# Kernel optimization log

Hardware: AMD Instinct MI355X
Metric: run time of the kernel (lower is better)

## Reference

```python
import jax, jax.numpy as jnp
import numpy as np

NHEAD = 8
ROUTING_STEPS = 2
TEMP = 1.0
ROPE_THETA = 10000.0


def rmsnorm(x, w, eps=1e-6):
    return x * jax.lax.rsqrt(jnp.mean(x * x, axis=-1, keepdims=True) + eps) * w


def rope_cos_sin(seq_len, head_dim, theta):
    inv = 1.0 / (theta ** (jnp.arange(0, head_dim, 2, dtype=jnp.float32) / head_dim))
    freqs = jnp.outer(jnp.arange(seq_len, dtype=jnp.float32), inv)  # [S, hd/2]
    return jnp.cos(freqs), jnp.sin(freqs)


def apply_rope(x, cos, sin):
    # x: [B,H,S,hd]; cos/sin: [S, hd/2]
    x1, x2 = x[..., 0::2], x[..., 1::2]
    c, s = cos[None, None], sin[None, None]
    r1 = x1 * c - x2 * s
    r2 = x1 * s + x2 * c
    return jnp.stack([r1, r2], axis=-1).reshape(x.shape)


def cube_forward(x, wq, wk, wv, wo, w1, w2, g1, g2, cos, sin):
    # Per-sample gathered expert weights: wq.. [B,D,D], w1 [B,D,F], w2 [B,F,D]
    B, S, D = x.shape
    H = NHEAD
    hd = D // H
    xn = rmsnorm(x, g1[:, None, :])
    q = jnp.einsum('bsd,bde->bse', xn, wq).reshape(B, S, H, hd).transpose(0, 2, 1, 3)
    k = jnp.einsum('bsd,bde->bse', xn, wk).reshape(B, S, H, hd).transpose(0, 2, 1, 3)
    v = jnp.einsum('bsd,bde->bse', xn, wv).reshape(B, S, H, hd).transpose(0, 2, 1, 3)
    q = apply_rope(q, cos, sin)
    k = apply_rope(k, cos, sin)
    scores = jnp.einsum('bhqd,bhkd->bhqk', q, k) / jnp.sqrt(jnp.float32(hd))
    causal = jnp.tril(jnp.ones((S, S), dtype=bool))
    scores = jnp.where(causal, scores, jnp.float32(-1e30))
    att = jax.nn.softmax(scores, axis=-1)
    o = jnp.einsum('bhqk,bhkd->bhqd', att, v).transpose(0, 2, 1, 3).reshape(B, S, D)
    x = x + jnp.einsum('bsd,bde->bse', o, wo)
    hn = rmsnorm(x, g2[:, None, :])
    ff = jax.nn.silu(jnp.einsum('bsd,bdf->bsf', hn, w1))
    return x + jnp.einsum('bsf,bfd->bsd', ff, w2)


def reference(input_ids, start_cubes, emb, Wq, Wk, Wv, Wo, W1, W2, n1, n2, gate_w, final_norm_w, fc_out_w):
    B, S = input_ids.shape
    D = emb.shape[1]
    C = Wq.shape[0]
    x = emb[input_ids] * jnp.sqrt(jnp.float32(D))
    cos, sin = rope_cos_sin(S, D // NHEAD, ROPE_THETA)
    # deterministic ring graph: neighbors of cube i are (i+1)%C and (i+2)%C
    ar = jnp.arange(C)
    adj = jnp.zeros((C, C), dtype=bool).at[ar, (ar + 1) % C].set(True).at[ar, (ar + 2) % C].set(True)
    cur = start_cubes
    acc_probs = jnp.zeros(C + 1, dtype=jnp.float32)
    acc_lb = jnp.float32(0.0)
    for _ in range(ROUTING_STEPS):
        x = cube_forward(x, Wq[cur], Wk[cur], Wv[cur], Wo[cur], W1[cur], W2[cur], n1[cur], n2[cur], cos, sin)
        pooled = x.mean(axis=1)                        # [B, D]
        scores = pooled @ gate_w                       # [B, C+1]
        probs = jax.nn.softmax(scores / TEMP, axis=-1)
        acc_probs = acc_probs + probs.sum(axis=0)
        avg = probs.mean(axis=0)
        acc_lb = acc_lb + (C + 1) * jnp.sum(avg * avg)
        masked = jnp.where(adj[cur], scores[:, :C], jnp.float32(-1e30))
        cur = jnp.argmax(masked, axis=-1)
    logits = jnp.einsum('bsd,dv->bsv', rmsnorm(x, final_norm_w), fc_out_w)
    avg_probs = acc_probs / jnp.float32(ROUTING_STEPS * B)
    aux_variance_loss = jnp.var(avg_probs)
    aux_lb_loss = acc_lb / jnp.float32(ROUTING_STEPS)
    return logits, aux_variance_loss, aux_lb_loss


def setup_inputs() -> dict:
    key = jax.random.key(0)
    ks = jax.random.split(key, 16)
    V, D, F, C, B, S = 32000, 512, 2048, 4, 2, 256
    w = 0.02
    return {
        'input_ids': jax.random.randint(ks[0], (B, S), 0, V),
        'start_cubes': jax.random.randint(ks[1], (B,), 0, C),
        'emb': jax.random.normal(ks[2], (V, D), jnp.float32) * w,
        'Wq': jax.random.normal(ks[3], (C, D, D), jnp.float32) * w,
        'Wk': jax.random.normal(ks[4], (C, D, D), jnp.float32) * w,
        'Wv': jax.random.normal(ks[5], (C, D, D), jnp.float32) * w,
        'Wo': jax.random.normal(ks[6], (C, D, D), jnp.float32) * w,
        'W1': jax.random.normal(ks[7], (C, D, F), jnp.float32) * w,
        'W2': jax.random.normal(ks[8], (C, F, D), jnp.float32) * w,
        'n1': jnp.ones((C, D), jnp.float32),
        'n2': jnp.ones((C, D), jnp.float32),
        'gate_w': jax.random.normal(ks[9], (D, C + 1), jnp.float32) * w,
        'final_norm_w': jnp.ones((D,), jnp.float32),
        'fc_out_w': jax.random.normal(ks[10], (D, V), jnp.float32) * w,
    }
```

## Files before the change

### kernel.cpp

```cpp
#include <hip/hip_runtime.h>
#include <hip/hip_bf16.h>

#define BB 2
#define SS 256
#define DDIM 512
#define HH 8
#define HDIM 64
#define FDIM 2048
#define CC 4
#define VV 32000
#define NTOK (BB*SS)
#define PCHUNK 16

typedef __hip_bfloat16 bf16;
typedef __attribute__((ext_vector_type(8))) short short8;
typedef __attribute__((ext_vector_type(4))) short short4v;
typedef __attribute__((ext_vector_type(4))) float floatx4;

__device__ __forceinline__ int get_mode(const unsigned* __restrict__ probe) {
    return (probe[0] == 0x3F800000u) ? 0 : 1;
}
__device__ __forceinline__ float ldw(const void* __restrict__ p, long i, int mode) {
    if (mode == 0) return ((const float*)p)[i];
    return __bfloat162float(((const bf16*)p)[i]);
}
__device__ __forceinline__ void stf(void* __restrict__ p, long i, float v, int mode) {
    if (mode == 0) ((float*)p)[i] = v;
    else ((bf16*)p)[i] = __float2bfloat16(v);
}

__device__ __forceinline__ void gload16(const void* g, void* l) {
    __builtin_amdgcn_global_load_lds(
        (const __attribute__((address_space(1))) unsigned int*)g,
        (__attribute__((address_space(3))) unsigned int*)l, 16, 0, 0);
}

__global__ void init_kernel(const int* __restrict__ ids,
                            const int* __restrict__ start_cubes,
                            const void* __restrict__ emb,
                            float* __restrict__ x,
                            float* __restrict__ acc_probs,
                            float* __restrict__ acc_lb,
                            int* __restrict__ cur,
                            const unsigned* __restrict__ probe) {
    int mode = get_mode(probe);
    int gid = blockIdx.x * blockDim.x + threadIdx.x;
    if (gid < NTOK * DDIM) {
        int tok = gid / DDIM, d = gid % DDIM;
        x[gid] = ldw(emb, (long)ids[tok] * DDIM + d, mode) * 22.627416997969522f;
    }
    if (gid < CC + 1) acc_probs[gid] = 0.f;
    if (gid == CC + 1) *acc_lb = 0.f;
    if (gid < BB) cur[gid] = start_cubes[gid];
}

__global__ void rmsnorm_kernel(const float* __restrict__ in,
                               void* __restrict__ out, int obf,
                               const void* __restrict__ gamma,
                               const int* __restrict__ cur,
                               float* __restrict__ zbuf, int zn,
                               const unsigned* __restrict__ probe) {
    int mode = get_mode(probe);
    int tok = blockIdx.x;
    int b = tok / SS;
    long goff = cur ? (long)cur[b] * DDIM : 0;
    if (zbuf) {
        int gtid = blockIdx.x * blockDim.x + threadIdx.x;
        int gstride = gridDim.x * blockDim.x;
        for (int i = gtid; i < zn; i += gstride) zbuf[i] = 0.f;
    }
    __shared__ float red[256];
    int t = threadIdx.x;
    float x0 = in[(long)tok * DDIM + t];
    float x1 = in[(long)tok * DDIM + t + 256];
    red[t] = x0 * x0 + x1 * x1;
    __syncthreads();
    for (int s = 128; s > 0; s >>= 1) {
        if (t < s) red[t] += red[t + s];
        __syncthreads();
    }
    float scale = rsqrtf(red[0] / DDIM + 1e-6f);
    float v0 = x0 * scale * ldw(gamma, goff + t, mode);
    float v1 = x1 * scale * ldw(gamma, goff + t + 256, mode);
    if (obf) {
        ((bf16*)out)[(long)tok * DDIM + t]       = __float2bfloat16(v0);
        ((bf16*)out)[(long)tok * DDIM + t + 256] = __float2bfloat16(v1);
    } else {
        ((float*)out)[(long)tok * DDIM + t]       = v0;
        ((float*)out)[(long)tok * DDIM + t + 256] = v1;
    }
}

__global__ void silu_kernel(const float* __restrict__ in,
                            ushort* __restrict__ out, int n) {
    int i4 = (blockIdx.x * blockDim.x + threadIdx.x) * 4;
    if (i4 >= n) return;
    float4 v = *(const float4*)&in[i4];
    float a = v.x / (1.f + expf(-v.x));
    float b = v.y / (1.f + expf(-v.y));
    float c = v.z / (1.f + expf(-v.z));
    float d = v.w / (1.f + expf(-v.w));
    bf16 t0 = __float2bfloat16(a), t1 = __float2bfloat16(b);
    bf16 t2 = __float2bfloat16(c), t3 = __float2bfloat16(d);
    short4v o;
    o[0] = *(short*)&t0; o[1] = *(short*)&t1;
    o[2] = *(short*)&t2; o[3] = *(short*)&t3;
    *(short4v*)&out[i4] = o;
}

__global__ void transpose_kernel(const void* __restrict__ in, bf16* __restrict__ out,
                                 int K, int N, long ims, long oms,
                                 const unsigned* __restrict__ probe) {
    int mode = get_mode(probe);
    __shared__ float tile[32][33];
    int mat = blockIdx.z;
    int n0 = blockIdx.x * 32, k0 = blockIdx.y * 32;
    int tx = threadIdx.x, ty = threadIdx.y;
#pragma unroll
    for (int i = 0; i < 4; i++)
        tile[ty + i * 8][tx] = ldw(in, (long)mat * ims + (long)(k0 + ty + i * 8) * N + (n0 + tx), mode);
    __syncthreads();
#pragma unroll
    for (int i = 0; i < 4; i++)
        out[(long)mat * oms + (long)(n0 + ty + i * 8) * K + (k0 + tx)] =
            __float2bfloat16(tile[tx][ty + i * 8]);
}

__global__ __launch_bounds__(256)
void gemm_mfma(const ushort* __restrict__ A,
               const ushort* __restrict__ WtB,
               const int* __restrict__ cur, long wcube, long wz,
               int K, int N,
               const float* __restrict__ res,
               void* __restrict__ out, long ozstride,
               int omode, int ACT, int nsplit, int swz,
               const unsigned* __restrict__ probe) {
    int mode = get_mode(probe);
    __shared__ __align__(16) ushort sA[2][128 * 32];
    __shared__ __align__(16) ushort sB[2][128 * 32];
    int tid = threadIdx.x;
    int mi = blockIdx.y, ni = blockIdx.x;
    if (swz) {
        int nb = gridDim.x, mb = gridDim.y;
        int lin = blockIdx.x + blockIdx.y * nb;
        int nwg = nb * mb;
        int q = nwg >> 3;
        int xcd = lin & 7, pos = lin >> 3;
        int nid = xcd * q + pos;
        mi = nid % mb;
        ni = nid / mb;
    }
    int m0 = mi * 128;
    int n0 = ni * 128;
    int z  = blockIdx.z / nsplit;
    int ks = blockIdx.z % nsplit;
    int Kc = K / nsplit;
    int kbeg = ks * Kc;
    const ushort* Wt = WtB + (long)z * wz + (cur ? (long)cur[m0 / SS] * wcube : 0);
    floatx4 acc[4][4];
#pragma unroll
    for (int i = 0; i < 4; i++)
#pragma unroll
        for (int j = 0; j < 4; j++)
#pragma unroll
            for (int r = 0; r < 4; r++) acc[i][j][r] = 0.f;
    int w = tid >> 6, lane = tid & 63;
    int wm = (w & 1) * 64, wn = (w >> 1) * 64;
    int lr = lane & 15, quad = lane >> 4;

    auto stage = [&](int buf, int k0) {
#pragma unroll
        for (int i = 0; i < 2; i++) {
            int g  = tid + i * 256;
            int gs = g ^ ((g >> 3) & 7);
            int rs = gs >> 2, cs = (gs & 3) * 8;
            gload16(&A[(long)(m0 + rs) * K + k0 + cs],  &sA[buf][g * 8]);
            gload16(&Wt[(long)(n0 + rs) * K + k0 + cs], &sB[buf][g * 8]);
        }
    };

    int nsteps = Kc >> 5;
    stage(0, kbeg);
    for (int j = 0; j < nsteps; ++j) {
        int cu = j & 1;
        if (j + 1 < nsteps) {
            stage(cu ^ 1, kbeg + ((j + 1) << 5));
            asm volatile("s_waitcnt vmcnt(4)" ::: "memory");
        } else {
            asm volatile("s_waitcnt vmcnt(0)" ::: "memory");
        }
        __builtin_amdgcn_sched_barrier(0);
        __builtin_amdgcn_s_barrier();
        short8 af[4], bfr[4];
#pragma unroll
        for (int i = 0; i < 4; i++) {
            int oA = (wm + i * 16 + lr) * 4 + quad;
            int sa = oA ^ ((oA >> 3) & 7);
            af[i]  = *(const short8*)&sA[cu][sa * 8];
            int oB = (wn + i * 16 + lr) * 4 + quad;
            int sb = oB ^ ((oB >> 3) & 7);
            bfr[i] = *(const short8*)&sB[cu][sb * 8];
        }
#pragma unroll
        for (int mm = 0; mm < 4; mm++)
#pragma unroll
            for (int nn = 0; nn < 4; nn++)
                acc[mm][nn] = __builtin_amdgcn_mfma_f32_16x16x32_bf16(af[mm], bfr[nn], acc[mm][nn], 0, 0, 0);
        asm volatile("s_waitcnt lgkmcnt(0)" ::: "memory");
        __builtin_amdgcn_sched_barrier(0);
        __builtin_amdgcn_s_barrier();
    }
#pragma unroll
    for (int mm = 0; mm < 4; mm++)
#pragma unroll
        for (int nn = 0; nn < 4; nn++) {
            int col = n0 + wn + nn * 16 + lr;
#pragma unroll
            for (int r = 0; r < 4; r++) {
                int row = m0 + wm + mm * 16 + quad * 4 + r;
                float v = acc[mm][nn][r];
                long oi = (long)z * ozstride + (long)row * N + col;
                if (omode == 3) {
                    atomicAdd((float*)out + oi, v);
                } else {
                    if (ACT == 1) v = v / (1.f + expf(-v));
                    if (res) v += res[(long)row * N + col];
                    if (omode == 0)      ((float*)out)[oi] = v;
                    else if (omode == 1) ((bf16*)out)[oi] = __float2bfloat16(v);
                    else                 stf(out, oi, v, mode);
                }
            }
        }
}

__global__ void rope_kernel(float* __restrict__ q, float* __restrict__ k) {
    int gid = blockIdx.x * blockDim.x + threadIdx.x;
    if (gid >= NTOK * HH * (HDIM / 2)) return;
    int j = gid % (HDIM / 2);
    int rest = gid / (HDIM / 2);
    int h = rest % HH;
    int tok = rest / HH;
    int s = tok % SS;
    float inv = expf(-(float)j * (logf(10000.f) / 32.f));
    float ang = (float)s * inv;
    float c = cosf(ang), sn = sinf(ang);
    long base = (long)tok * DDIM + h * HDIM + 2 * j;
    float q1 = q[base], q2 = q[base + 1];
    q[base]     = q1 * c - q2 * sn;
    q[base + 1] = q1 * sn + q2 * c;
    float k1 = k[base], k2 = k[base + 1];
    k[base]     = k1 * c - k2 * sn;
    k[base + 1] = k1 * sn + k2 * c;
}

__global__ void attn_kernel(const float* __restrict__ q,
                            const float* __restrict__ k,
                            const float* __restrict__ v,
                            void* __restrict__ o, int obf) {
    int blk = blockIdx.x;
    int qr = blk % SS;
    int h = (blk / SS) % HH;
    int b = blk / (SS * HH);
    int t = threadIdx.x;
    __shared__ float sc[256];
    __shared__ float red[256];
    __shared__ __align__(16) float qs[HDIM];
    long qbase = ((long)(b * SS + qr)) * DDIM + h * HDIM;
    if (t < HDIM) qs[t] = q[qbase + t];
    __syncthreads();
    float s = -1e30f;
    if (t <= qr) {
        long kbase = ((long)(b * SS + t)) * DDIM + h * HDIM;
        const float4* k4 = (const float4*)&k[kbase];
        const float4* q4 = (const float4*)qs;
        float acc = 0.f;
#pragma unroll
        for (int i = 0; i < HDIM / 4; i++) {
            float4 a = q4[i], bv = k4[i];
            acc += a.x * bv.x + a.y * bv.y + a.z * bv.z + a.w * bv.w;
        }
        s = acc * 0.125f;
    }
    sc[t] = s;
    red[t] = s;
    __syncthreads();
    for (int st = 128; st > 0; st >>= 1) {
        if (t < st) red[t] = fmaxf(red[t], red[t + st]);
        __syncthreads();
    }
    float m = red[0];
    __syncthreads();
    float e = (t <= qr) ? expf(sc[t] - m) : 0.f;
    sc[t] = e;
    red[t] = e;
    __syncthreads();
    for (int st = 128; st > 0; st >>= 1) {
        if (t < st) red[t] += red[t + st];
        __syncthreads();
    }
    float invsum = 1.f / red[0];
    __syncthreads();
    int g = t >> 6, d = t & 63;
    float pacc = 0.f;
    for (int kk = g; kk <= qr; kk += 4)
        pacc += sc[kk] * v[((long)(b * SS + kk)) * DDIM + h * HDIM + d];
    red[t] = pacc;
    __syncthreads();
    if (t < HDIM) {
        float vv = (red[t] + red[t + 64] + red[t + 128] + red[t + 192]) * invsum;
        if (obf) ((bf16*)o)[qbase + t] = __float2bfloat16(vv);
        else     ((float*)o)[qbase + t] = vv;
    }
}

__global__ void pool_partial_kernel(const float* __restrict__ x,
                                    float* __restrict__ partial) {
    int blk = blockIdx.x;
    int b = blk / (SS / PCHUNK);
    int c = blk % (SS / PCHUNK);
    int t = threadIdx.x;
    float acc = 0.f;
    long base = ((long)b * SS + c * PCHUNK) * DDIM + t;
#pragma unroll
    for (int i = 0; i < PCHUNK; i++) acc += x[base + (long)i * DDIM];
    partial[(long)blk * DDIM + t] = acc;
}

__global__ void routing_kernel(const float* __restrict__ partial,
                               const void* __restrict__ gate_w,
                               float* __restrict__ acc_probs,
                               float* __restrict__ acc_lb,
                               int* __restrict__ cur,
                               int final_step,
                               void* __restrict__ d_out,
                               const unsigned* __restrict__ probe) {
    int mode = get_mode(probe);
    __shared__ float pooled[BB][DDIM];
    __shared__ float scores[BB][CC + 1];
    int t = threadIdx.x;
#pragma unroll
    for (int b = 0; b < BB; b++) {
        float acc = 0.f;
#pragma unroll
        for (int c = 0; c < SS / PCHUNK; c++)
            acc += partial[((long)b * (SS / PCHUNK) + c) * DDIM + t];
        pooled[b][t] = acc / (float)SS;
    }
    __syncthreads();
    if (t < BB * (CC + 1)) {
        int b = t / (CC + 1), c = t % (CC + 1);
        float acc = 0.f;
        for (int d = 0; d < DDIM; d++)
            acc += pooled[b][d] * ldw(gate_w, (long)d * (CC + 1) + c, mode);
        scores[b][c] = acc;
    }
    __syncthreads();
    if (t == 0) {
        float probs[BB][CC + 1];
        for (int b = 0; b < BB; b++) {
            float m = -1e30f;
            for (int c = 0; c <= CC; c++) m = fmaxf(m, scores[b][c]);
            float sum = 0.f;
            for (int c = 0; c <= CC; c++) { probs[b][c] = expf(scores[b][c] - m); sum += probs[b][c]; }
            for (int c = 0; c <= CC; c++) probs[b][c] /= sum;
        }
        float lb = 0.f;
        for (int c = 0; c <= CC; c++) {
            float sumb = 0.f;
            for (int b = 0; b < BB; b++) sumb += probs[b][c];
            acc_probs[c] += sumb;
            float avg = sumb / (float)BB;
            lb += avg * avg;
        }
        *acc_lb += (float)(CC + 1) * lb;
        for (int b = 0; b < BB; b++) {
            int cu = cur[b];
            int a1 = (cu + 1) % CC, a2 = (cu + 2) % CC;
            float best = -1e38f; int bi = 0;
            for (int c = 0; c < CC; c++) {
                float vv = (c == a1 || c == a2) ? scores[b][c] : -1e30f;
                if (vv > best) { best = vv; bi = c; }
            }
            cur[b] = bi;
        }
        if (final_step) {
            float ap[CC + 1], mean = 0.f;
            for (int c = 0; c <= CC; c++) { ap[c] = acc_probs[c] / (2.f * BB); mean += ap[c]; }
            mean /= (float)(CC + 1);
            float var = 0.f;
            for (int c = 0; c <= CC; c++) { float d = ap[c] - mean; var += d * d; }
            var /= (float)(CC + 1);
            stf(d_out, (long)NTOK * VV + 0, var, mode);
            stf(d_out, (long)NTOK * VV + 1, (*acc_lb) / 2.f, mode);
        }
    }
}

template <int TM, int ACT, bool OUT_DYN>
__global__ void gemm_kernel(const float* __restrict__ A,
                            const void* __restrict__ Wbase,
                            const int* __restrict__ cur, long wstride,
                            int K, int N,
                            const float* __restrict__ res,
                            void* __restrict__ out,
                            const unsigned* __restrict__ probe) {
    int mode = get_mode(probe);
    extern __shared__ float sA[];
    int row0 = blockIdx.y * TM;
    long woff = cur ? (long)cur[row0 / SS] * wstride : 0;
    int t = threadIdx.x;
    for (int i = t; i < TM * K; i += 256)
        sA[i] = A[(long)(row0 + i / K) * K + (i % K)];
    __syncthreads();
    int n = blockIdx.x * 256 + t;
    float acc[TM];
#pragma unroll
    for (int r = 0; r < TM; r++) acc[r] = 0.f;
    for (int k = 0; k < K; k++) {
        float w = ldw(Wbase, woff + (long)k * N + n, mode);
#pragma unroll
        for (int r = 0; r < TM; r++) acc[r] += sA[r * K + k] * w;
    }
#pragma unroll
    for (int r = 0; r < TM; r++) {
        float v = acc[r];
        if (ACT == 1) v = v / (1.f + expf(-v));
        if (res) v += res[(long)(row0 + r) * N + n];
        long oi = (long)(row0 + r) * N + n;
        if constexpr (OUT_DYN) stf(out, oi, v, mode);
        else                   ((float*)out)[oi] = v;
    }
}

__global__ void routing_kernel_fb(const float* __restrict__ x,
                                  const void* __restrict__ gate_w,
                                  float* __restrict__ acc_probs,
                                  float* __restrict__ acc_lb,
                                  int* __restrict__ cur,
                                  int final_step,
                                  void* __restrict__ d_out,
                                  const unsigned* __restrict__ probe) {
    int mode = get_mode(probe);
    __shared__ float pooled[BB][DDIM];
    __shared__ float scores[BB][CC + 1];
    int t = threadIdx.x;
    for (int b = 0; b < BB; b++) {
        float acc = 0.f;
        for (int s = 0; s < SS; s++) acc += x[((long)(b * SS + s)) * DDIM + t];
        pooled[b][t] = acc / (float)SS;
    }
    __syncthreads();
    if (t < BB * (CC + 1)) {
        int b = t / (CC + 1), c = t % (CC + 1);
        float acc = 0.f;
        for (int d = 0; d < DDIM; d++)
            acc += pooled[b][d] * ldw(gate_w, (long)d * (CC + 1) + c, mode);
        scores[b][c] = acc;
    }
    __syncthreads();
    if (t == 0) {
        float probs[BB][CC + 1];
        for (int b = 0; b < BB; b++) {
            float m = -1e30f;
            for (int c = 0; c <= CC; c++) m = fmaxf(m, scores[b][c]);
            float sum = 0.f;
            for (int c = 0; c <= CC; c++) { probs[b][c] = expf(scores[b][c] - m); sum += probs[b][c]; }
            for (int c = 0; c <= CC; c++) probs[b][c] /= sum;
        }
        float lb = 0.f;
        for (int c = 0; c <= CC; c++) {
            float sumb = 0.f;
            for (int b = 0; b < BB; b++) sumb += probs[b][c];
            acc_probs[c] += sumb;
            float avg = sumb / (float)BB;
            lb += avg * avg;
        }
        *acc_lb += (float)(CC + 1) * lb;
        for (int b = 0; b < BB; b++) {
            int cu = cur[b];
            int a1 = (cu + 1) % CC, a2 = (cu + 2) % CC;
            float best = -1e38f; int bi = 0;
            for (int c = 0; c < CC; c++) {
                float vv = (c == a1 || c == a2) ? scores[b][c] : -1e30f;
                if (vv > best) { best = vv; bi = c; }
            }
            cur[b] = bi;
        }
        if (final_step) {
            float ap[CC + 1], mean = 0.f;
            for (int c = 0; c <= CC; c++) { ap[c] = acc_probs[c] / (2.f * BB); mean += ap[c]; }
            mean /= (float)(CC + 1);
            float var = 0.f;
            for (int c = 0; c <= CC; c++) { float d = ap[c] - mean; var += d * d; }
            var /= (float)(CC + 1);
            stf(d_out, (long)NTOK * VV + 0, var, mode);
            stf(d_out, (long)NTOK * VV + 1, (*acc_lb) / 2.f, mode);
        }
    }
}

extern "C" void kernel_launch(void* const* d_in, const int* in_sizes, int n_in,
                              void* d_out, int out_size, void* d_ws, size_t ws_size,
                              hipStream_t stream) {
    const int*  ids   = (const int*)d_in[0];
    const int*  start = (const int*)d_in[1];
    const void* emb   = d_in[2];
    const void* Wq    = d_in[3];
    const void* Wk    = d_in[4];
    const void* Wv    = d_in[5];
    const void* Wo    = d_in[6];
    const void* W1    = d_in[7];
    const void* W2    = d_in[8];
    const void* n1    = d_in[9];
    const void* n2    = d_in[10];
    const void* gate  = d_in[11];
    const void* fnorm = d_in[12];
    const void* fcw   = d_in[13];
    const unsigned* probe = (const unsigned*)d_in[9];

    char* base = (char*)d_ws;
    size_t off = 0;
    auto alloc = [&](size_t bytes) { size_t p = off; off = (off + bytes + 255) & ~(size_t)255; return p; };
    size_t x_o    = alloc((size_t)NTOK * DDIM * 4);
    size_t qkv_o  = alloc((size_t)3 * NTOK * DDIM * 4);
    size_t xn_o   = alloc((size_t)NTOK * DDIM * 2);
    size_t ob_o   = alloc((size_t)NTOK * DDIM * 2);
    size_t ff_o   = alloc((size_t)NTOK * FDIM * 2);
    size_t ffp_o  = alloc((size_t)NTOK * FDIM * 4);
    size_t acc_o  = alloc(256);
    size_t part_o = alloc((size_t)BB * (SS / PCHUNK) * DDIM * 4);
    size_t qkvT_o = alloc((size_t)3 * CC * DDIM * DDIM * 2);
    size_t WoT_o  = alloc((size_t)CC * DDIM * DDIM * 2);
    size_t W1T_o  = alloc((size_t)CC * DDIM * FDIM * 2);
    size_t W2T_o  = alloc((size_t)CC * FDIM * DDIM * 2);
    size_t fcwT_o = alloc((size_t)DDIM * VV * 2);
    bool big = ws_size >= off;

    if (big) {
        float* x    = (float*)(base + x_o);
        float* qkv  = (float*)(base + qkv_o);
        float* q = qkv, *k = qkv + NTOK * DDIM, *v = qkv + 2 * NTOK * DDIM;
        bf16*  xn   = (bf16*)(base + xn_o);
        bf16*  ob   = (bf16*)(base + ob_o);
        bf16*  ff   = (bf16*)(base + ff_o);
        float* ffp  = (float*)(base + ffp_o);
        float* acc_probs = (float*)(base + acc_o);
        float* acc_lb = acc_probs + 8;
        int*   cur = (int*)(acc_lb + 8);
        float* partial = (float*)(base + part_o);
        bf16* qkvT = (bf16*)(base + qkvT_o);
        bf16* WoT  = (bf16*)(base + WoT_o);
        bf16* W1T  = (bf16*)(base + W1T_o);
        bf16* W2T  = (bf16*)(base + W2T_o);
        bf16* fcwT = (bf16*)(base + fcwT_o);

        dim3 tb(32, 8);
        transpose_kernel<<<dim3(16, 16, CC), tb, 0, stream>>>(Wq, qkvT,                 DDIM, DDIM, (long)DDIM*DDIM, (long)DDIM*DDIM, probe);
        transpose_kernel<<<dim3(16, 16, CC), tb, 0, stream>>>(Wk, qkvT +   CC*DDIM*DDIM, DDIM, DDIM, (long)DDIM*DDIM, (long)DDIM*DDIM, probe);
        transpose_kernel<<<dim3(16, 16, CC), tb, 0, stream>>>(Wv, qkvT + 2*CC*DDIM*DDIM, DDIM, DDIM, (long)DDIM*DDIM, (long)DDIM*DDIM, probe);
        transpose_kernel<<<dim3(16, 16, CC), tb, 0, stream>>>(Wo, WoT,  DDIM, DDIM, (long)DDIM*DDIM, (long)DDIM*DDIM, probe);
        transpose_kernel<<<dim3(64, 16, CC), tb, 0, stream>>>(W1, W1T,  DDIM, FDIM, (long)DDIM*FDIM, (long)FDIM*DDIM, probe);
        transpose_kernel<<<dim3(16, 64, CC), tb, 0, stream>>>(W2, W2T,  FDIM, DDIM, (long)FDIM*DDIM, (long)DDIM*FDIM, probe);
        transpose_kernel<<<dim3(1000, 16, 1), tb, 0, stream>>>(fcw, fcwT, DDIM, VV, 0, 0, probe);

        init_kernel<<<(NTOK * DDIM + 255) / 256, 256, 0, stream>>>(
            ids, start, emb, x, acc_probs, acc_lb, cur, probe);

        const long DD2 = (long)DDIM * DDIM;
        const int QS = 4;
        const int OS = 4;
        const int F1S = 4;
        const int F2S = 8;
        for (int step = 0; step < 2; step++) {
            rmsnorm_kernel<<<NTOK, 256, 0, stream>>>(x, xn, 1, n1, cur,
                                                     qkv, 3 * NTOK * DDIM, probe);
            gemm_mfma<<<dim3(DDIM/128, NTOK/128, 3*QS), 256, 0, stream>>>(
                (const ushort*)xn, (const ushort*)qkvT, cur, DD2, (long)CC*DD2,
                DDIM, DDIM, nullptr, qkv, (long)NTOK*DDIM, 3, 0, QS, 0, probe);
            rope_kernel<<<(NTOK * HH * (HDIM / 2) + 255) / 256, 256, 0, stream>>>(q, k);
            attn_kernel<<<BB * HH * SS, 256, 0, stream>>>(q, k, v, ob, 1);
            gemm_mfma<<<dim3(DDIM/128, NTOK/128, OS), 256, 0, stream>>>(
                (const ushort*)ob, (const ushort*)WoT, cur, DD2, 0,
                DDIM, DDIM, nullptr, x, 0, 3, 0, OS, 0, probe);
            rmsnorm_kernel<<<NTOK, 256, 0, stream>>>(x, xn, 1, n2, cur,
                                                     ffp, NTOK * FDIM, probe);
            gemm_mfma<<<dim3(FDIM/128, NTOK/128, F1S), 256, 0, stream>>>(
                (const ushort*)xn, (const ushort*)W1T, cur, (long)FDIM*DDIM, 0,
                DDIM, FDIM, nullptr, ffp, 0, 3, 0, F1S, 0, probe);
            silu_kernel<<<(NTOK * FDIM / 4 + 255) / 256, 256, 0, stream>>>(
                ffp, (ushort*)ff, NTOK * FDIM);
            gemm_mfma<<<dim3(DDIM/128, NTOK/128, F2S), 256, 0, stream>>>(
                (const ushort*)ff, (const ushort*)W2T, cur, (long)DDIM*FDIM, 0,
                FDIM, DDIM, nullptr, x, 0, 3, 0, F2S, 0, probe);
            pool_partial_kernel<<<BB * (SS / PCHUNK), 512, 0, stream>>>(x, partial);
            routing_kernel<<<1, 512, 0, stream>>>(
                partial, gate, acc_probs, acc_lb, cur, step == 1, d_out, probe);
        }
        rmsnorm_kernel<<<NTOK, 256, 0, stream>>>(x, xn, 1, fnorm, nullptr,
                                                 nullptr, 0, probe);
        gemm_mfma<<<dim3(VV/128, NTOK/128, 1), 256, 0, stream>>>(
            (const ushort*)xn, (const ushort*)fcwT, nullptr, 0, 0,
            DDIM, VV, nullptr, d_out, 0, 2, 0, 1, 1, probe);
        return;
    }

    float* ws = (float*)d_ws;
    float* x  = ws;
    float* xn = x  + NTOK * DDIM;
    float* q  = xn + NTOK * DDIM;
    float* k  = q  + NTOK * DDIM;
    float* v  = k  + NTOK * DDIM;
    float* o  = v  + NTOK * DDIM;
    float* ff = o  + NTOK * DDIM;
    float* acc_probs = ff + NTOK * FDIM;
    float* acc_lb    = acc_probs + 8;
    int*   cur       = (int*)(acc_lb + 8);
    const long DD2 = (long)DDIM * DDIM;

    init_kernel<<<(NTOK * DDIM + 255) / 256, 256, 0, stream>>>(
        ids, start, emb, x, acc_probs, acc_lb, cur, probe);
    for (int step = 0; step < 2; step++) {
        rmsnorm_kernel<<<NTOK, 256, 0, stream>>>(x, xn, 0, n1, cur, nullptr, 0, probe);
        dim3 gdd(DDIM / 256, NTOK / 16);
        size_t smem16 = 16 * DDIM * sizeof(float);
        gemm_kernel<16, 0, false><<<gdd, 256, smem16, stream>>>(
            xn, Wq, cur, DD2, DDIM, DDIM, nullptr, q, probe);
        gemm_kernel<16, 0, false><<<gdd, 256, smem16, stream>>>(
            xn, Wk, cur, DD2, DDIM, DDIM, nullptr, k, probe);
        gemm_kernel<16, 0, false><<<gdd, 256, smem16, stream>>>(
            xn, Wv, cur, DD2, DDIM, DDIM, nullptr, v, probe);
        rope_kernel<<<(NTOK * HH * (HDIM / 2) + 255) / 256, 256, 0, stream>>>(q, k);
        attn_kernel<<<BB * HH * SS, 256, 0, stream>>>(q, k, v, o, 0);
        gemm_kernel<16, 0, false><<<gdd, 256, smem16, stream>>>(
            o, Wo, cur, DD2, DDIM, DDIM, x, x, probe);
        rmsnorm_kernel<<<NTOK, 256, 0, stream>>>(x, xn, 0, n2, cur, nullptr, 0, probe);
        dim3 gdf(FDIM / 256, NTOK / 16);
        gemm_kernel<16, 1, false><<<gdf, 256, smem16, stream>>>(
            xn, W1, cur, (long)DDIM * FDIM, DDIM, FDIM, nullptr, ff, probe);
        dim3 gfd(DDIM / 256, NTOK / 4);
        size_t smem4f = 4 * FDIM * sizeof(float);
        gemm_kernel<4, 0, false><<<gfd, 256, smem4f, stream>>>(
            ff, W2, cur, (long)FDIM * DDIM, FDIM, DDIM, x, x, probe);
        routing_kernel_fb<<<1, 512, 0, stream>>>(
            x, gate, acc_probs, acc_lb, cur, step == 1, d_out, probe);
    }
    rmsnorm_kernel<<<NTOK, 256, 0, stream>>>(x, xn, 0, fnorm, nullptr, nullptr, 0, probe);
    dim3 gv(VV / 256, NTOK / 16);
    size_t smem16 = 16 * DDIM * sizeof(float);
    gemm_kernel<16, 0, true><<<gv, 256, smem16, stream>>>(
        xn, fcw, nullptr, 0, DDIM, VV, nullptr, d_out, probe);
}
```

Baseline: 594.2 us.

## Triple-buffer GEMM LDS staging and parallelize routing gate reduction

The MFMA GEMM moves from double to triple buffering of the A/B LDS tiles. It prefetches two K-steps ahead and relaxes the vmcnt waits so more global loads are in flight. Separately, the routing kernel stops having 10 threads serially loop over 512 dims for the gate projection. Every thread now computes its partial products, reduces them with wave shuffles, and thread 0 sums the per-wave results. The extra LDS (48KB per block) may reduce occupancy.

```diff
diff --git a/kernel.cpp b/kernel.cpp
--- a/kernel.cpp
+++ b/kernel.cpp
@@ -136,8 +136,8 @@
                int omode, int ACT, int nsplit, int swz,
                const unsigned* __restrict__ probe) {
     int mode = get_mode(probe);
-    __shared__ __align__(16) ushort sA[2][128 * 32];
-    __shared__ __align__(16) ushort sB[2][128 * 32];
+    __shared__ __align__(16) ushort sA[3][128 * 32];
+    __shared__ __align__(16) ushort sB[3][128 * 32];
     int tid = threadIdx.x;
     int mi = blockIdx.y, ni = blockIdx.x;
     if (swz) {
@@ -181,10 +181,13 @@
 
     int nsteps = Kc >> 5;
     stage(0, kbeg);
+    if (nsteps > 1) stage(1, kbeg + 32);
     for (int j = 0; j < nsteps; ++j) {
-        int cu = j & 1;
-        if (j + 1 < nsteps) {
-            stage(cu ^ 1, kbeg + ((j + 1) << 5));
+        int cu = j % 3;
+        if (j + 2 < nsteps) {
+            stage((j + 2) % 3, kbeg + ((j + 2) << 5));
+            asm volatile("s_waitcnt vmcnt(8)" ::: "memory");
+        } else if (j + 1 < nsteps) {
             asm volatile("s_waitcnt vmcnt(4)" ::: "memory");
         } else {
             asm volatile("s_waitcnt vmcnt(0)" ::: "memory");
@@ -335,27 +338,47 @@
                                void* __restrict__ d_out,
                                const unsigned* __restrict__ probe) {
     int mode = get_mode(probe);
-    __shared__ float pooled[BB][DDIM];
+    __shared__ float wred[8][BB * (CC + 1)];
     __shared__ float scores[BB][CC + 1];
     int t = threadIdx.x;
+    float pm[BB];
 #pragma unroll
     for (int b = 0; b < BB; b++) {
         float acc = 0.f;
 #pragma unroll
         for (int c = 0; c < SS / PCHUNK; c++)
             acc += partial[((long)b * (SS / PCHUNK) + c) * DDIM + t];
-        pooled[b][t] = acc / (float)SS;
-    }
-    __syncthreads();
-    if (t < BB * (CC + 1)) {
-        int b = t / (CC + 1), c = t % (CC + 1);
-        float acc = 0.f;
-        for (int d = 0; d < DDIM; d++)
-            acc += pooled[b][d] * ldw(gate_w, (long)d * (CC + 1) + c, mode);
-        scores[b][c] = acc;
-    }
+        pm[b] = acc / (float)SS;
+    }
+    float part[BB][CC + 1];
+#pragma unroll
+    for (int c = 0; c <= CC; c++) {
+        float g = ldw(gate_w, (long)t * (CC + 1) + c, mode);
+#pragma unroll
+        for (int b = 0; b < BB; b++) part[b][c] = pm[b] * g;
+    }
+#pragma unroll
+    for (int off = 32; off > 0; off >>= 1)
+#pragma unroll
+        for (int b = 0; b < BB; b++)
+#pragma unroll
+            for (int c = 0; c <= CC; c++)
+                part[b][c] += __shfl_down(part[b][c], off);
+    int wave = t >> 6, lane = t & 63;
+    if (lane == 0)
+#pragma unroll
+        for (int b = 0; b < BB; b++)
+#pragma unroll
+            for (int c = 0; c <= CC; c++)
+                wred[wave][b * (CC + 1) + c] = part[b][c];
     __syncthreads();
     if (t == 0) {
+        for (int b = 0; b < BB; b++)
+            for (int c = 0; c <= CC; c++) {
+                float s = 0.f;
+                for (int wv = 0; wv < 8; wv++) s += wred[wv][b * (CC + 1) + c];
+                scores[b][c] = s;
+            }
         float probs[BB][CC + 1];
         for (int b = 0; b < BB; b++) {
             float m = -1e30f;
```

Result: faster. 513.1 us (-13.7%).
